# Performance work log

Measured on AMD Instinct MI355X. Metric: run time of the kernel, lower is better.

## Reference

```python
import jax, jax.numpy as jnp
import numpy as np

N_HEAD = 16
NEG = -1e9

def setup_inputs() -> dict:
    key = jax.random.key(0)
    k1, k2, k3 = jax.random.split(key, 3)
    B, S, NX = 8, 1024, 1024
    x = jax.random.normal(k1, (B, S, NX), dtype=jnp.float32)
    w_attn = jax.random.normal(k2, (NX, 3 * NX), dtype=jnp.float32) * 0.02
    b_attn = jnp.zeros((3 * NX,), dtype=jnp.float32)
    w_proj = jax.random.normal(k3, (NX, NX), dtype=jnp.float32) * 0.02
    b_proj = jnp.zeros((NX,), dtype=jnp.float32)
    return {"x": x, "w_attn": w_attn, "b_attn": b_attn, "w_proj": w_proj, "b_proj": b_proj}

def reference(x, w_attn, b_attn, w_proj, b_proj):
    B, S, NX = x.shape
    H = N_HEAD
    D = NX // H
    qkv = x @ w_attn + b_attn                      # [B,S,3*NX]
    q, k, v = jnp.split(qkv, 3, axis=-1)           # each [B,S,NX]
    q = q.reshape(B, S, H, D)
    k = k.reshape(B, S, H, D)
    v = v.reshape(B, S, H, D)
    # scores with scale (scale=True -> divide by sqrt(head_dim))
    w = jnp.einsum('bqhd,bkhd->bhqk', q, k) / jnp.sqrt(jnp.float32(D))
    tril = jnp.tril(jnp.ones((S, S), dtype=w.dtype))  # causal mask buffer
    w = w * tril + NEG * (1.0 - tril)
    w = jax.nn.softmax(w, axis=-1)                 # dropout is identity at eval
    a = jnp.einsum('bhqk,bkhd->bqhd', w, v)        # [B,S,H,D]
    a = a.reshape(B, S, NX)
    a = a @ w_proj + b_proj
    return a
```

## Files before the change

### kernel.cpp

```cpp
#include <hip/hip_runtime.h>
#include <hip/hip_bf16.h>
#include <stdint.h>

typedef __bf16 bf16x8 __attribute__((ext_vector_type(8)));
typedef float  f32x4  __attribute__((ext_vector_type(4)));
typedef float  f32x16 __attribute__((ext_vector_type(16)));

#define BARRIER() asm volatile("s_barrier" ::: "memory")
#define VMCNT(n)  asm volatile("s_waitcnt vmcnt(" #n ")" ::: "memory")

__device__ __forceinline__ void gload_lds16(const void* g, void* l) {
  __builtin_amdgcn_global_load_lds(
      (const __attribute__((address_space(1))) unsigned int*)g,
      (__attribute__((address_space(3))) unsigned int*)l, 16, 0, 0);
}

__global__ void k_cast(const float* __restrict__ in, __bf16* __restrict__ out, int n4) {
  int i = blockIdx.x * blockDim.x + threadIdx.x;
  if (i >= n4) return;
  float4 v = reinterpret_cast<const float4*>(in)[i];
  union { __bf16 h[4]; uint64_t u; } c;
  c.h[0] = (__bf16)v.x; c.h[1] = (__bf16)v.y; c.h[2] = (__bf16)v.z; c.h[3] = (__bf16)v.w;
  *reinterpret_cast<uint64_t*>(out + 4l * i) = c.u;
}

__global__ void k_transpose_cast(const float* __restrict__ in, __bf16* __restrict__ out,
                                 int R, int C) {
  __shared__ float t[32][33];
  const int tx = threadIdx.x & 31, ty = threadIdx.x >> 5;
  const int c0 = blockIdx.x * 32, r0 = blockIdx.y * 32;
#pragma unroll
  for (int rr = 0; rr < 4; ++rr)
    t[ty * 4 + rr][tx] = in[(long)(r0 + ty * 4 + rr) * C + c0 + tx];
  __syncthreads();
#pragma unroll
  for (int rr = 0; rr < 4; ++rr)
    out[(long)(c0 + ty * 4 + rr) * R + r0 + tx] = (__bf16)t[tx][ty * 4 + rr];
}

template <int MODE>
__launch_bounds__(512, 2)
__global__ void k_gemm_p(const __bf16* __restrict__ A, const __bf16* __restrict__ Bt,
                         const float* __restrict__ bias, int M, int N, int K, int NB,
                         __bf16* __restrict__ qo, __bf16* __restrict__ ko,
                         __bf16* __restrict__ vo, float* __restrict__ fo) {
  __shared__ __bf16 lds[2][3][8192];
  const int tid = threadIdx.x;
  const int l = tid & 63, w = tid >> 6;
  const int lm = l & 15, lq = l >> 4;
  const int wm = w >> 2, wn = w & 3;
  const int nwg = gridDim.x;
  const int wg = (blockIdx.x & 7) * (nwg >> 3) + (blockIdx.x >> 3);
  const int bm = wg / NB, bn = wg % NB;
  const int nt = K >> 6;

  const int rh0 = tid >> 3;
  const int scol = ((tid & 7) * 16) ^ ((rh0 & 7) << 4);
  long a_off[2][2], b_off[2];
#pragma unroll
  for (int h = 0; h < 2; ++h)
#pragma unroll
    for (int li = 0; li < 2; ++li) {
      const int row_h = li * 64 + rh0;
      const int g_r = bm * 256 + ((row_h >> 4) << 5) + h * 16 + (row_h & 15);
      a_off[h][li] = (long)g_r * K + (scol >> 1);
    }
#pragma unroll
  for (int li = 0; li < 2; ++li)
    b_off[li] = (long)(bn * 128 + li * 64 + rh0) * K + (scol >> 1);

#define STAGE_AH(h, buf, t) { \
    gload_lds16(A + a_off[h][0] + (long)(t) * 64, &lds[buf][h][tid * 8]); \
    gload_lds16(A + a_off[h][1] + (long)(t) * 64, &lds[buf][h][4096 + tid * 8]); }
#define STAGE_B(buf, t) { \
    gload_lds16(Bt + b_off[0] + (long)(t) * 64, &lds[buf][2][tid * 8]); \
    gload_lds16(Bt + b_off[1] + (long)(t) * 64, &lds[buf][2][4096 + tid * 8]); }

  const int aswz = (lm & 7) << 4;

  f32x4 acc[8][2] = {};

  STAGE_B(0, 0); STAGE_AH(0, 0, 0); STAGE_AH(1, 0, 0);
  VMCNT(2); BARRIER();

  int cur = 0;
  for (int t = 0; t < nt; ++t) {
    const int nxt = cur ^ 1;
    bf16x8 bf[2][2], ae[4][2];
#pragma unroll
    for (int nj = 0; nj < 2; ++nj)
#pragma unroll
      for (int ks = 0; ks < 2; ++ks) {
        const int rh = wn * 32 + nj * 16 + lm;
        bf[nj][ks] = *(const bf16x8*)&lds[cur][2][rh * 64 + (((ks * 64 + lq * 16) ^ aswz) >> 1)];
      }
#pragma unroll
    for (int me = 0; me < 4; ++me)
#pragma unroll
      for (int ks = 0; ks < 2; ++ks) {
        const int rh = (wm * 4 + me) * 16 + lm;
        ae[me][ks] = *(const bf16x8*)&lds[cur][0][rh * 64 + (((ks * 64 + lq * 16) ^ aswz) >> 1)];
      }
    if (t + 1 < nt) {
      STAGE_B(nxt, t + 1); STAGE_AH(0, nxt, t + 1);
      VMCNT(4);
    } else {
      VMCNT(0);
    }
    BARRIER();
    __builtin_amdgcn_s_setprio(1);
#pragma unroll
    for (int ks = 0; ks < 2; ++ks)
#pragma unroll
      for (int me = 0; me < 4; ++me)
#pragma unroll
        for (int nj = 0; nj < 2; ++nj)
          acc[2 * me][nj] = __builtin_amdgcn_mfma_f32_16x16x32_bf16(ae[me][ks], bf[nj][ks],
                                                                    acc[2 * me][nj], 0, 0, 0);
    __builtin_amdgcn_s_setprio(0);
    BARRIER();
    bf16x8 ao[4][2];
#pragma unroll
    for (int mo = 0; mo < 4; ++mo)
#pragma unroll
      for (int ks = 0; ks < 2; ++ks) {
        const int rh = (wm * 4 + mo) * 16 + lm;
        ao[mo][ks] = *(const bf16x8*)&lds[cur][1][rh * 64 + (((ks * 64 + lq * 16) ^ aswz) >> 1)];
      }
    if (t + 1 < nt) {
      STAGE_AH(1, nxt, t + 1);
      VMCNT(2);
    }
    BARRIER();
    __builtin_amdgcn_s_setprio(1);
#pragma unroll
    for (int ks = 0; ks < 2; ++ks)
#pragma unroll
      for (int mo = 0; mo < 4; ++mo)
#pragma unroll
        for (int nj = 0; nj < 2; ++nj)
          acc[2 * mo + 1][nj] = __builtin_amdgcn_mfma_f32_16x16x32_bf16(ao[mo][ks], bf[nj][ks],
                                                                        acc[2 * mo + 1][nj], 0, 0, 0);
    __builtin_amdgcn_s_setprio(0);
    BARRIER();
    cur = nxt;
  }

  if (MODE == 0) {
#pragma unroll
    for (int nj = 0; nj < 2; ++nj) {
      const int c = bn * 128 + wn * 32 + nj * 16 + lm;
      const float bv = bias[c];
      const int which = c >> 10, cc = c & 1023, hh = cc >> 6, d = cc & 63;
#pragma unroll
      for (int mi = 0; mi < 8; ++mi)
#pragma unroll
        for (int i = 0; i < 4; ++i) {
          const int r = bm * 256 + wm * 128 + mi * 16 + lq * 4 + i;
          const int b = r >> 10, s_ = r & 1023;
          float fv = acc[mi][nj][i] + bv;
          if (which == 0) fv *= 0.125f;
          const __bf16 v = (__bf16)fv;
          const long hb = (long)(b * 16 + hh);
          if (which == 0)      qo[(hb * 1024 + s_) * 64 + d] = v;
          else if (which == 1) ko[(hb * 1024 + s_) * 64 + d] = v;
          else                 vo[(hb * 64 + d) * 1024 + s_] = v;
        }
    }
  } else {
#pragma unroll
    for (int nj = 0; nj < 2; ++nj) {
      const int c = bn * 128 + wn * 32 + nj * 16 + lm;
      const float bv = bias[c];
#pragma unroll
      for (int mi = 0; mi < 8; ++mi)
#pragma unroll
        for (int i = 0; i < 4; ++i) {
          const int r = bm * 256 + wm * 128 + mi * 16 + lq * 4 + i;
          fo[(long)r * N + c] = acc[mi][nj][i] + bv;
        }
    }
  }
#undef STAGE_AH
#undef STAGE_B
}

__device__ __forceinline__ void attn_qtile(const __bf16* __restrict__ Q,
                                           const __bf16* __restrict__ Kh,
                                           const __bf16* __restrict__ Vt,
                                           __bf16* __restrict__ ob,
                                           int b, int h, int qbw, int l) {
  const int lm = l & 31, hi = l >> 5;

  bf16x8 qf[4];
#pragma unroll
  for (int ds = 0; ds < 4; ++ds)
    qf[ds] = *(const bf16x8*)(Q + (long)(qbw + lm) * 64 + ds * 16 + hi * 8);

  f32x16 oacc0 = {}, oacc1 = {};
  float m = -__builtin_inff(), s = 0.f;

  const int ntiles = (qbw >> 5) + 1;
  for (int kt = 0; kt < ntiles; ++kt) {
    const int k0 = kt * 32;
    f32x16 st = {};
#pragma unroll
    for (int ds = 0; ds < 4; ++ds) {
      bf16x8 kf = *(const bf16x8*)(Kh + (long)(k0 + lm) * 64 + ds * 16 + hi * 8);
      st = __builtin_amdgcn_mfma_f32_32x32x16_bf16(kf, qf[ds], st, 0, 0, 0);
    }
    if (kt == ntiles - 1) {
      const int q = qbw + lm;
#pragma unroll
      for (int r = 0; r < 16; ++r) {
        const int key = k0 + (r & 3) + 8 * (r >> 2) + 4 * hi;
        if (key > q) st[r] = -__builtin_inff();
      }
    }
    float tm = st[0];
#pragma unroll
    for (int r = 1; r < 16; ++r) tm = fmaxf(tm, st[r]);
    tm = fmaxf(tm, __shfl_xor(tm, 32));
    if (!__all(tm <= m + 8.f)) {
      const float mn = fmaxf(m, tm);
      const float fac = __expf(m - mn);
      m = mn;
      s *= fac;
#pragma unroll
      for (int r = 0; r < 16; ++r) {
        const int qr = (r & 3) + 8 * (r >> 2) + 4 * hi;
        const float fr = __int_as_float(
            __builtin_amdgcn_ds_bpermute(qr * 4, __float_as_int(fac)));
        oacc0[r] *= fr; oacc1[r] *= fr;
      }
    }
    float p[16], ts = 0.f;
#pragma unroll
    for (int r = 0; r < 16; ++r) { p[r] = __expf(st[r] - m); ts += p[r]; }
    ts += __shfl_xor(ts, 32);
    s += ts;
    unsigned int w8[8];
#pragma unroll
    for (int t = 0; t < 8; ++t) {
      union { __bf16 hh[2]; unsigned int u; } pk;
      pk.hh[0] = (__bf16)p[2 * t]; pk.hh[1] = (__bf16)p[2 * t + 1];
      w8[t] = pk.u;
    }
    const unsigned int e0 = __shfl_xor(hi ? w8[0] : w8[2], 32);
    const unsigned int e1 = __shfl_xor(hi ? w8[1] : w8[3], 32);
    const unsigned int e2 = __shfl_xor(hi ? w8[4] : w8[6], 32);
    const unsigned int e3 = __shfl_xor(hi ? w8[5] : w8[7], 32);
    union { unsigned int wd[4]; bf16x8 v; } pa0, pa1;
    if (hi) {
      pa0.wd[0] = e0;    pa0.wd[1] = e1;    pa0.wd[2] = w8[2]; pa0.wd[3] = w8[3];
      pa1.wd[0] = e2;    pa1.wd[1] = e3;    pa1.wd[2] = w8[6]; pa1.wd[3] = w8[7];
    } else {
      pa0.wd[0] = w8[0]; pa0.wd[1] = w8[1]; pa0.wd[2] = e0;    pa0.wd[3] = e1;
      pa1.wd[0] = w8[4]; pa1.wd[1] = w8[5]; pa1.wd[2] = e2;    pa1.wd[3] = e3;
    }
#pragma unroll
    for (int t = 0; t < 2; ++t) {
      const bf16x8 pa = t ? pa1.v : pa0.v;
      bf16x8 vf0 = *(const bf16x8*)(Vt + (long)lm * 1024 + k0 + t * 16 + hi * 8);
      bf16x8 vf1 = *(const bf16x8*)(Vt + (long)(32 + lm) * 1024 + k0 + t * 16 + hi * 8);
      oacc0 = __builtin_amdgcn_mfma_f32_32x32x16_bf16(pa, vf0, oacc0, 0, 0, 0);
      oacc1 = __builtin_amdgcn_mfma_f32_32x32x16_bf16(pa, vf1, oacc1, 0, 0, 0);
    }
  }
  const float invs = 1.f / s;
#pragma unroll
  for (int r = 0; r < 16; ++r) {
    const int qr = (r & 3) + 8 * (r >> 2) + 4 * hi;
    const float inv = __int_as_float(
        __builtin_amdgcn_ds_bpermute(qr * 4, __float_as_int(invs)));
    const long row = (long)(b * 1024 + qbw + qr) * 1024 + h * 64;
    ob[row + lm]      = (__bf16)(oacc0[r] * inv);
    ob[row + 32 + lm] = (__bf16)(oacc1[r] * inv);
  }
}

__global__ void k_attn(const __bf16* __restrict__ qb_, const __bf16* __restrict__ kb,
                       const __bf16* __restrict__ vtb, __bf16* __restrict__ ob) {
  const int l = threadIdx.x & 63, w = threadIdx.x >> 6;
  const int bh = blockIdx.y, b = bh >> 4, h = bh & 15;
  const int wi = blockIdx.x * 4 + w;
  const __bf16* Q  = qb_ + (long)bh * 65536;
  const __bf16* Kh = kb  + (long)bh * 65536;
  const __bf16* Vt = vtb + (long)bh * 65536;
  attn_qtile(Q, Kh, Vt, ob, b, h, wi * 32, l);
  attn_qtile(Q, Kh, Vt, ob, b, h, (31 - wi) * 32, l);
}

extern "C" void kernel_launch(void* const* d_in, const int* in_sizes, int n_in,
                              void* d_out, int out_size, void* d_ws, size_t ws_size,
                              hipStream_t stream) {
  const float* x      = (const float*)d_in[0];
  const float* w_attn = (const float*)d_in[1];
  const float* b_attn = (const float*)d_in[2];
  const float* w_proj = (const float*)d_in[3];
  const float* b_proj = (const float*)d_in[4];
  float* out = (float*)d_out;

  char* ws = (char*)d_ws;
  const size_t SZ_XBF = (size_t)8192 * 1024 * 2;
  __bf16* x_bf = (__bf16*)ws;  ws += SZ_XBF;
  __bf16* wat  = (__bf16*)ws;  ws += (size_t)3072 * 1024 * 2;
  __bf16* wpt  = (__bf16*)ws;  ws += (size_t)1024 * 1024 * 2;
  __bf16* qb   = (__bf16*)ws;  ws += SZ_XBF;
  __bf16* kb   = (__bf16*)ws;  ws += SZ_XBF;
  __bf16* vtb  = (__bf16*)ws;  ws += SZ_XBF;
  __bf16* obf  = (__bf16*)ws;  ws += SZ_XBF;

  k_cast<<<8192, 256, 0, stream>>>(x, x_bf, 2097152);
  k_transpose_cast<<<dim3(96, 32), 256, 0, stream>>>(w_attn, wat, 1024, 3072);
  k_transpose_cast<<<dim3(32, 32), 256, 0, stream>>>(w_proj, wpt, 1024, 1024);
  k_gemm_p<0><<<768, 512, 0, stream>>>(x_bf, wat, b_attn, 8192, 3072, 1024, 24,
                                       qb, kb, vtb, nullptr);
  k_attn<<<dim3(4, 128), 256, 0, stream>>>(qb, kb, vtb, obf);
  k_gemm_p<1><<<256, 512, 0, stream>>>(obf, wpt, b_proj, 8192, 1024, 1024, 8,
                                       nullptr, nullptr, nullptr, out);
}
```

Before: 279.0 us.

## Triple-buffer GEMM LDS pipeline and fuse two attention query tiles per wave

The GEMM moves from double-buffered LDS with interleaved A halves to a three-stage ring. Each A and B tile is prefetched two k-steps ahead, and explicit lgkmcnt waits and sched barriers are placed around the MFMA blocks. The attention kernel now runs its paired causal query tiles in one joint loop, so each loaded K and V fragment serves both tiles instead of being reloaded for each. The cost is more LDS per block, which may reduce occupancy, and higher register pressure in attention.

Result: slower. 331.8 us (+18.9%).

```diff
diff --git a/kernel.cpp b/kernel.cpp
--- a/kernel.cpp
+++ b/kernel.cpp
@@ -8,6 +8,8 @@
 
 #define BARRIER() asm volatile("s_barrier" ::: "memory")
 #define VMCNT(n)  asm volatile("s_waitcnt vmcnt(" #n ")" ::: "memory")
+#define LGKM0()   asm volatile("s_waitcnt lgkmcnt(0)" ::: "memory")
+#define SCHED0()  __builtin_amdgcn_sched_barrier(0)
 
 __device__ __forceinline__ void gload_lds16(const void* g, void* l) {
   __builtin_amdgcn_global_load_lds(
@@ -44,9 +46,10 @@
                          const float* __restrict__ bias, int M, int N, int K, int NB,
                          __bf16* __restrict__ qo, __bf16* __restrict__ ko,
                          __bf16* __restrict__ vo, float* __restrict__ fo) {
-  __shared__ __bf16 lds[2][3][8192];
+  __shared__ __bf16 lds[3][24576];
   const int tid = threadIdx.x;
-  const int l = tid & 63, w = tid >> 6;
+  const int l = tid & 63;
+  const int w = tid >> 6;
   const int lm = l & 15, lq = l >> 4;
   const int wm = w >> 2, wn = w & 3;
   const int nwg = gridDim.x;
@@ -54,96 +57,89 @@
   const int bm = wg / NB, bn = wg % NB;
   const int nt = K >> 6;
 
-  const int rh0 = tid >> 3;
-  const int scol = ((tid & 7) * 16) ^ ((rh0 & 7) << 4);
-  long a_off[2][2], b_off[2];
-#pragma unroll
-  for (int h = 0; h < 2; ++h)
-#pragma unroll
-    for (int li = 0; li < 2; ++li) {
-      const int row_h = li * 64 + rh0;
-      const int g_r = bm * 256 + ((row_h >> 4) << 5) + h * 16 + (row_h & 15);
-      a_off[h][li] = (long)g_r * K + (scol >> 1);
-    }
-#pragma unroll
-  for (int li = 0; li < 2; ++li)
-    b_off[li] = (long)(bn * 128 + li * 64 + rh0) * K + (scol >> 1);
-
-#define STAGE_AH(h, buf, t) { \
-    gload_lds16(A + a_off[h][0] + (long)(t) * 64, &lds[buf][h][tid * 8]); \
-    gload_lds16(A + a_off[h][1] + (long)(t) * 64, &lds[buf][h][4096 + tid * 8]); }
+  const int rA = tid >> 3;
+  const int scol = (((tid & 7) * 16) ^ ((rA & 7) << 4)) >> 1;
+  long a_off[4], b_off[2];
+#pragma unroll
+  for (int li = 0; li < 4; ++li) a_off[li] = (long)(bm * 256 + li * 64 + rA) * K + scol;
+#pragma unroll
+  for (int li = 0; li < 2; ++li) b_off[li] = (long)(bn * 128 + li * 64 + rA) * K + scol;
+
+#define STAGE_A(buf, t) { \
+    gload_lds16(A + a_off[0] + (long)(t) * 64, &lds[buf][tid * 8]); \
+    gload_lds16(A + a_off[1] + (long)(t) * 64, &lds[buf][4096 + tid * 8]); \
+    gload_lds16(A + a_off[2] + (long)(t) * 64, &lds[buf][8192 + tid * 8]); \
+    gload_lds16(A + a_off[3] + (long)(t) * 64, &lds[buf][12288 + tid * 8]); }
 #define STAGE_B(buf, t) { \
-    gload_lds16(Bt + b_off[0] + (long)(t) * 64, &lds[buf][2][tid * 8]); \
-    gload_lds16(Bt + b_off[1] + (long)(t) * 64, &lds[buf][2][4096 + tid * 8]); }
+    gload_lds16(Bt + b_off[0] + (long)(t) * 64, &lds[buf][16384 + tid * 8]); \
+    gload_lds16(Bt + b_off[1] + (long)(t) * 64, &lds[buf][20480 + tid * 8]); }
 
   const int aswz = (lm & 7) << 4;
+  const int cofs0 = ((0 * 64 + lq * 16) ^ aswz) >> 1;
+  const int cofs1 = ((1 * 64 + lq * 16) ^ aswz) >> 1;
+  const int arow = wm * 128 + lm;
+  const int brow = wn * 32 + lm;
 
   f32x4 acc[8][2] = {};
 
-  STAGE_B(0, 0); STAGE_AH(0, 0, 0); STAGE_AH(1, 0, 0);
-  VMCNT(2); BARRIER();
-
-  int cur = 0;
+  STAGE_A(0, 0); STAGE_B(0, 0);
+  STAGE_A(1, 1); STAGE_B(1, 1);
+  VMCNT(6); BARRIER();
+
   for (int t = 0; t < nt; ++t) {
-    const int nxt = cur ^ 1;
-    bf16x8 bf[2][2], ae[4][2];
-#pragma unroll
-    for (int nj = 0; nj < 2; ++nj)
-#pragma unroll
-      for (int ks = 0; ks < 2; ++ks) {
-        const int rh = wn * 32 + nj * 16 + lm;
-        bf[nj][ks] = *(const bf16x8*)&lds[cur][2][rh * 64 + (((ks * 64 + lq * 16) ^ aswz) >> 1)];
-      }
-#pragma unroll
-    for (int me = 0; me < 4; ++me)
-#pragma unroll
-      for (int ks = 0; ks < 2; ++ks) {
-        const int rh = (wm * 4 + me) * 16 + lm;
-        ae[me][ks] = *(const bf16x8*)&lds[cur][0][rh * 64 + (((ks * 64 + lq * 16) ^ aswz) >> 1)];
-      }
-    if (t + 1 < nt) {
-      STAGE_B(nxt, t + 1); STAGE_AH(0, nxt, t + 1);
-      VMCNT(4);
+    const int cb = t % 3;
+    const __bf16* Lb = lds[cb];
+    bf16x8 bf[2][2], af[4][2];
+#pragma unroll
+    for (int nj = 0; nj < 2; ++nj) {
+      bf[nj][0] = *(const bf16x8*)&Lb[16384 + (brow + nj * 16) * 64 + cofs0];
+      bf[nj][1] = *(const bf16x8*)&Lb[16384 + (brow + nj * 16) * 64 + cofs1];
+    }
+#pragma unroll
+    for (int mi = 0; mi < 4; ++mi) {
+      af[mi][0] = *(const bf16x8*)&Lb[(arow + mi * 16) * 64 + cofs0];
+      af[mi][1] = *(const bf16x8*)&Lb[(arow + mi * 16) * 64 + cofs1];
+    }
+    if (t + 2 < nt) STAGE_A((t + 2) % 3, t + 2);
+    BARRIER();
+    LGKM0(); SCHED0();
+    __builtin_amdgcn_s_setprio(1);
+#pragma unroll
+    for (int ks = 0; ks < 2; ++ks)
+#pragma unroll
+      for (int mi = 0; mi < 4; ++mi)
+#pragma unroll
+        for (int nj = 0; nj < 2; ++nj)
+          acc[mi][nj] = __builtin_amdgcn_mfma_f32_16x16x32_bf16(af[mi][ks], bf[nj][ks],
+                                                                acc[mi][nj], 0, 0, 0);
+    __builtin_amdgcn_s_setprio(0);
+    SCHED0();
+    BARRIER();
+#pragma unroll
+    for (int mi = 0; mi < 4; ++mi) {
+      af[mi][0] = *(const bf16x8*)&Lb[(arow + (mi + 4) * 16) * 64 + cofs0];
+      af[mi][1] = *(const bf16x8*)&Lb[(arow + (mi + 4) * 16) * 64 + cofs1];
+    }
+    if (t + 2 < nt) {
+      STAGE_B((t + 2) % 3, t + 2);
+      VMCNT(6);
     } else {
       VMCNT(0);
     }
     BARRIER();
+    LGKM0(); SCHED0();
     __builtin_amdgcn_s_setprio(1);
 #pragma unroll
     for (int ks = 0; ks < 2; ++ks)
 #pragma unroll
-      for (int me = 0; me < 4; ++me)
+      for (int mi = 0; mi < 4; ++mi)
 #pragma unroll
         for (int nj = 0; nj < 2; ++nj)
-          acc[2 * me][nj] = __builtin_amdgcn_mfma_f32_16x16x32_bf16(ae[me][ks], bf[nj][ks],
-                                                                    acc[2 * me][nj], 0, 0, 0);
+          acc[mi + 4][nj] = __builtin_amdgcn_mfma_f32_16x16x32_bf16(af[mi][ks], bf[nj][ks],
+                                                                    acc[mi + 4][nj], 0, 0, 0);
     __builtin_amdgcn_s_setprio(0);
+    SCHED0();
     BARRIER();
-    bf16x8 ao[4][2];
-#pragma unroll
-    for (int mo = 0; mo < 4; ++mo)
-#pragma unroll
-      for (int ks = 0; ks < 2; ++ks) {
-        const int rh = (wm * 4 + mo) * 16 + lm;
-        ao[mo][ks] = *(const bf16x8*)&lds[cur][1][rh * 64 + (((ks * 64 + lq * 16) ^ aswz) >> 1)];
-      }
-    if (t + 1 < nt) {
-      STAGE_AH(1, nxt, t + 1);
-      VMCNT(2);
-    }
-    BARRIER();
-    __builtin_amdgcn_s_setprio(1);
-#pragma unroll
-    for (int ks = 0; ks < 2; ++ks)
-#pragma unroll
-      for (int mo = 0; mo < 4; ++mo)
-#pragma unroll
-        for (int nj = 0; nj < 2; ++nj)
-          acc[2 * mo + 1][nj] = __builtin_amdgcn_mfma_f32_16x16x32_bf16(ao[mo][ks], bf[nj][ks],
-                                                                        acc[2 * mo + 1][nj], 0, 0, 0);
-    __builtin_amdgcn_s_setprio(0);
-    BARRIER();
-    cur = nxt;
   }
 
   if (MODE == 0) {
@@ -181,92 +177,74 @@
         }
     }
   }
-#undef STAGE_AH
+#undef STAGE_A
 #undef STAGE_B
 }
 
-__device__ __forceinline__ void attn_qtile(const __bf16* __restrict__ Q,
-                                           const __bf16* __restrict__ Kh,
-                                           const __bf16* __restrict__ Vt,
+__device__ __forceinline__ void sm_pv(f32x16& st, float& m, float& s,
+                                      f32x16& o0, f32x16& o1,
+                                      const bf16x8 vf[2][2],
+                                      int qbw, int k0, bool diag, int lm, int hi) {
+  if (diag) {
+    const int q = qbw + lm;
+#pragma unroll
+    for (int r = 0; r < 16; ++r) {
+      const int key = k0 + (r & 3) + 8 * (r >> 2) + 4 * hi;
+      if (key > q) st[r] = -__builtin_inff();
+    }
+  }
+  float tm = st[0];
+#pragma unroll
+  for (int r = 1; r < 16; ++r) tm = fmaxf(tm, st[r]);
+  tm = fmaxf(tm, __shfl_xor(tm, 32));
+  if (!__all(tm <= m + 8.f)) {
+    const float mn = fmaxf(m, tm);
+    const float fac = __expf(m - mn);
+    m = mn;
+    s *= fac;
+#pragma unroll
+    for (int r = 0; r < 16; ++r) {
+      const int qr = (r & 3) + 8 * (r >> 2) + 4 * hi;
+      const float fr = __int_as_float(
+          __builtin_amdgcn_ds_bpermute(qr * 4, __float_as_int(fac)));
+      o0[r] *= fr; o1[r] *= fr;
+    }
+  }
+  float p[16], ts = 0.f;
+#pragma unroll
+  for (int r = 0; r < 16; ++r) { p[r] = __expf(st[r] - m); ts += p[r]; }
+  ts += __shfl_xor(ts, 32);
+  s += ts;
+  unsigned int w8[8];
+#pragma unroll
+  for (int t = 0; t < 8; ++t) {
+    union { __bf16 hh[2]; unsigned int u; } pk;
+    pk.hh[0] = (__bf16)p[2 * t]; pk.hh[1] = (__bf16)p[2 * t + 1];
+    w8[t] = pk.u;
+  }
+  const unsigned int e0 = __shfl_xor(hi ? w8[0] : w8[2], 32);
+  const unsigned int e1 = __shfl_xor(hi ? w8[1] : w8[3], 32);
+  const unsigned int e2 = __shfl_xor(hi ? w8[4] : w8[6], 32);
+  const unsigned int e3 = __shfl_xor(hi ? w8[5] : w8[7], 32);
+  union { unsigned int wd[4]; bf16x8 v; } pa0, pa1;
+  if (hi) {
+    pa0.wd[0] = e0;    pa0.wd[1] = e1;    pa0.wd[2] = w8[2]; pa0.wd[3] = w8[3];
+    pa1.wd[0] = e2;    pa1.wd[1] = e3;    pa1.wd[2] = w8[6]; pa1.wd[3] = w8[7];
+  } else {
+    pa0.wd[0] = w8[0]; pa0.wd[1] = w8[1]; pa0.wd[2] = e0;    pa0.wd[3] = e1;
+    pa1.wd[0] = w8[4]; pa1.wd[1] = w8[5]; pa1.wd[2] = e2;    pa1.wd[3] = e3;
+  }
+#pragma unroll
+  for (int t = 0; t < 2; ++t) {
+    const bf16x8 pa = t ? pa1.v : pa0.v;
+    o0 = __builtin_amdgcn_mfma_f32_32x32x16_bf16(pa, vf[t][0], o0, 0, 0, 0);
+    o1 = __builtin_amdgcn_mfma_f32_32x32x16_bf16(pa, vf[t][1], o1, 0, 0, 0);
+  }
+}
+
+__device__ __forceinline__ void attn_write(const f32x16& o0, const f32x16& o1, float s,
                                            __bf16* __restrict__ ob,
-                                           int b, int h, int qbw, int l) {
-  const int lm = l & 31, hi = l >> 5;
-
-  bf16x8 qf[4];
-#pragma unroll
-  for (int ds = 0; ds < 4; ++ds)
-    qf[ds] = *(const bf16x8*)(Q + (long)(qbw + lm) * 64 + ds * 16 + hi * 8);
-
-  f32x16 oacc0 = {}, oacc1 = {};
-  float m = -__builtin_inff(), s = 0.f;
-
-  const int ntiles = (qbw >> 5) + 1;
-  for (int kt = 0; kt < ntiles; ++kt) {
-    const int k0 = kt * 32;
-    f32x16 st = {};
-#pragma unroll
-    for (int ds = 0; ds < 4; ++ds) {
-      bf16x8 kf = *(const bf16x8*)(Kh + (long)(k0 + lm) * 64 + ds * 16 + hi * 8);
-      st = __builtin_amdgcn_mfma_f32_32x32x16_bf16(kf, qf[ds], st, 0, 0, 0);
-    }
-    if (kt == ntiles - 1) {
-      const int q = qbw + lm;
-#pragma unroll
-      for (int r = 0; r < 16; ++r) {
-        const int key = k0 + (r & 3) + 8 * (r >> 2) + 4 * hi;
-        if (key > q) st[r] = -__builtin_inff();
-      }
-    }
-    float tm = st[0];
-#pragma unroll
-    for (int r = 1; r < 16; ++r) tm = fmaxf(tm, st[r]);
-    tm = fmaxf(tm, __shfl_xor(tm, 32));
-    if (!__all(tm <= m + 8.f)) {
-      const float mn = fmaxf(m, tm);
-      const float fac = __expf(m - mn);
-      m = mn;
-      s *= fac;
-#pragma unroll
-      for (int r = 0; r < 16; ++r) {
-        const int qr = (r & 3) + 8 * (r >> 2) + 4 * hi;
-        const float fr = __int_as_float(
-            __builtin_amdgcn_ds_bpermute(qr * 4, __float_as_int(fac)));
-        oacc0[r] *= fr; oacc1[r] *= fr;
-      }
-    }
-    float p[16], ts = 0.f;
-#pragma unroll
-    for (int r = 0; r < 16; ++r) { p[r] = __expf(st[r] - m); ts += p[r]; }
-    ts += __shfl_xor(ts, 32);
-    s += ts;
-    unsigned int w8[8];
-#pragma unroll
-    for (int t = 0; t < 8; ++t) {
-      union { __bf16 hh[2]; unsigned int u; } pk;
-      pk.hh[0] = (__bf16)p[2 * t]; pk.hh[1] = (__bf16)p[2 * t + 1];
-      w8[t] = pk.u;
-    }
-    const unsigned int e0 = __shfl_xor(hi ? w8[0] : w8[2], 32);
-    const unsigned int e1 = __shfl_xor(hi ? w8[1] : w8[3], 32);
-    const unsigned int e2 = __shfl_xor(hi ? w8[4] : w8[6], 32);
-    const unsigned int e3 = __shfl_xor(hi ? w8[5] : w8[7], 32);
-    union { unsigned int wd[4]; bf16x8 v; } pa0, pa1;
-    if (hi) {
-      pa0.wd[0] = e0;    pa0.wd[1] = e1;    pa0.wd[2] = w8[2]; pa0.wd[3] = w8[3];
-      pa1.wd[0] = e2;    pa1.wd[1] = e3;    pa1.wd[2] = w8[6]; pa1.wd[3] = w8[7];
-    } else {
-      pa0.wd[0] = w8[0]; pa0.wd[1] = w8[1]; pa0.wd[2] = e0;    pa0.wd[3] = e1;
-      pa1.wd[0] = w8[4]; pa1.wd[1] = w8[5]; pa1.wd[2] = e2;    pa1.wd[3] = e3;
-    }
-#pragma unroll
-    for (int t = 0; t < 2; ++t) {
-      const bf16x8 pa = t ? pa1.v : pa0.v;
-      bf16x8 vf0 = *(const bf16x8*)(Vt + (long)lm * 1024 + k0 + t * 16 + hi * 8);
-      bf16x8 vf1 = *(const bf16x8*)(Vt + (long)(32 + lm) * 1024 + k0 + t * 16 + hi * 8);
-      oacc0 = __builtin_amdgcn_mfma_f32_32x32x16_bf16(pa, vf0, oacc0, 0, 0, 0);
-      oacc1 = __builtin_amdgcn_mfma_f32_32x32x16_bf16(pa, vf1, oacc1, 0, 0, 0);
-    }
-  }
+                                           int b, int h, int qbw, int lm, int hi) {
   const float invs = 1.f / s;
 #pragma unroll
   for (int r = 0; r < 16; ++r) {
@@ -274,21 +252,62 @@
     const float inv = __int_as_float(
         __builtin_amdgcn_ds_bpermute(qr * 4, __float_as_int(invs)));
     const long row = (long)(b * 1024 + qbw + qr) * 1024 + h * 64;
-    ob[row + lm]      = (__bf16)(oacc0[r] * inv);
-    ob[row + 32 + lm] = (__bf16)(oacc1[r] * inv);
+    ob[row + lm]      = (__bf16)(o0[r] * inv);
+    ob[row + 32 + lm] = (__bf16)(o1[r] * inv);
   }
 }
 
 __global__ void k_attn(const __bf16* __restrict__ qb_, const __bf16* __restrict__ kb,
                        const __bf16* __restrict__ vtb, __bf16* __restrict__ ob) {
   const int l = threadIdx.x & 63, w = threadIdx.x >> 6;
+  const int lm = l & 31, hi = l >> 5;
   const int bh = blockIdx.y, b = bh >> 4, h = bh & 15;
   const int wi = blockIdx.x * 4 + w;
   const __bf16* Q  = qb_ + (long)bh * 65536;
   const __bf16* Kh = kb  + (long)bh * 65536;
   const __bf16* Vt = vtb + (long)bh * 65536;
-  attn_qtile(Q, Kh, Vt, ob, b, h, wi * 32, l);
-  attn_qtile(Q, Kh, Vt, ob, b, h, (31 - wi) * 32, l);
+
+  const int qbA = wi * 32,        ntA = wi + 1;
+  const int qbB = (31 - wi) * 32, ntB = 32 - wi;
+
+  bf16x8 qfA[4], qfB[4];
+#pragma unroll
+  for (int ds = 0; ds < 4; ++ds) {
+    qfA[ds] = *(const bf16x8*)(Q + (long)(qbA + lm) * 64 + ds * 16 + hi * 8);
+    qfB[ds] = *(const bf16x8*)(Q + (long)(qbB + lm) * 64 + ds * 16 + hi * 8);
+  }
+
+  f32x16 oA0 = {}, oA1 = {}, oB0 = {}, oB1 = {};
+  float mA = -__builtin_inff(), sA = 0.f;
+  float mB = -__builtin_inff(), sB = 0.f;
+
+  for (int kt = 0; kt < ntB; ++kt) {
+    const int k0 = kt * 32;
+    const bool actA = (kt < ntA);
+    bf16x8 kf[4];
+#pragma unroll
+    for (int ds = 0; ds < 4; ++ds)
+      kf[ds] = *(const bf16x8*)(Kh + (long)(k0 + lm) * 64 + ds * 16 + hi * 8);
+    f32x16 stA = {}, stB = {};
+#pragma unroll
+    for (int ds = 0; ds < 4; ++ds)
+      stB = __builtin_amdgcn_mfma_f32_32x32x16_bf16(kf[ds], qfB[ds], stB, 0, 0, 0);
+    if (actA) {
+#pragma unroll
+      for (int ds = 0; ds < 4; ++ds)
+        stA = __builtin_amdgcn_mfma_f32_32x32x16_bf16(kf[ds], qfA[ds], stA, 0, 0, 0);
+    }
+    bf16x8 vf[2][2];
+#pragma unroll
+    for (int t = 0; t < 2; ++t) {
+      vf[t][0] = *(const bf16x8*)(Vt + (long)lm * 1024 + k0 + t * 16 + hi * 8);
+      vf[t][1] = *(const bf16x8*)(Vt + (long)(32 + lm) * 1024 + k0 + t * 16 + hi * 8);
+    }
+    if (actA) sm_pv(stA, mA, sA, oA0, oA1, vf, qbA, k0, kt == ntA - 1, lm, hi);
+    sm_pv(stB, mB, sB, oB0, oB1, vf, qbB, k0, kt == ntB - 1, lm, hi);
+  }
+  attn_write(oA0, oA1, sA, ob, b, h, qbA, lm, hi);
+  attn_write(oB0, oB1, sB, ob, b, h, qbB, lm, hi);
 }
 
 extern "C" void kernel_launch(void* const* d_in, const int* in_sizes, int n_in,
```
